# Kernel optimization log

Measured on AMD Instinct MI355X. Metric: run time of the kernel, lower is better.

The kernel has to match this reference:

```python
import jax, jax.numpy as jnp
import numpy as np

N_NODES = 50000
N_EDGES = 800000
N_GRAPHS = 64
F_IN, F_HID, F_OUT = 128, 128, 16


def _graph_conv(x, W, b, src, dst, activation=None):
    """DGL GraphConv with norm='both': D_out^{-1/2} A^T D_in^{-1/2} X W + b."""
    n = x.shape[0]
    ones = jnp.ones((src.shape[0],), dtype=x.dtype)
    deg_out = jnp.clip(jax.ops.segment_sum(ones, src, num_segments=n), 1.0)
    deg_in = jnp.clip(jax.ops.segment_sum(ones, dst, num_segments=n), 1.0)
    h = x * jax.lax.rsqrt(deg_out)[:, None]          # scale by src out-degree
    agg = jax.ops.segment_sum(h[src], dst, num_segments=n)  # gather+scatter-add
    agg = agg * jax.lax.rsqrt(deg_in)[:, None]       # scale by dst in-degree
    out = agg @ W + b
    if activation is not None:
        out = activation(out)
    return out


def setup_inputs() -> dict:
    key = jax.random.key(0)
    ks = jax.random.split(key, 6)
    x = jax.random.normal(ks[0], (N_NODES, F_IN), dtype=jnp.float32)
    W1 = jax.random.normal(ks[1], (F_IN, F_HID), dtype=jnp.float32) * (F_IN ** -0.5)
    b1 = jnp.zeros((F_HID,), dtype=jnp.float32)
    W2 = jax.random.normal(ks[2], (F_HID, F_OUT), dtype=jnp.float32) * (F_HID ** -0.5)
    b2 = jnp.zeros((F_OUT,), dtype=jnp.float32)
    src = jax.random.randint(ks[3], (N_EDGES,), 0, N_NODES, dtype=jnp.int32)
    dst = jax.random.randint(ks[4], (N_EDGES,), 0, N_NODES, dtype=jnp.int32)
    graph_ids = jnp.sort(jax.random.randint(ks[5], (N_NODES,), 0, N_GRAPHS, dtype=jnp.int32))
    return {"x": x, "W1": W1, "b1": b1, "W2": W2, "b2": b2,
            "src": src, "dst": dst, "graph_ids": graph_ids}


def reference(x, W1, b1, W2, b2, src, dst, graph_ids):
    h = _graph_conv(x, W1, b1, src, dst, activation=jax.nn.relu)
    h = _graph_conv(h, W2, b2, src, dst, activation=None)
    # dgl.mean_nodes: per-graph mean over nodes
    sums = jax.ops.segment_sum(h, graph_ids, num_segments=N_GRAPHS)
    counts = jnp.clip(jax.ops.segment_sum(jnp.ones((N_NODES,), h.dtype), graph_ids,
                                          num_segments=N_GRAPHS), 1.0)
    return sums / counts[:, None]
```

## Files before the change

### kernel.cpp

```cpp
#include <hip/hip_runtime.h>
#include <hip/hip_bf16.h>

#define N_NODES_C 50000
#define N_EDGES_C 800000
#define N_GRAPHS_C 64
#define NBKT 782
#define BKTP 784
#define CHUNK 4096
#define NBLK_E 196

typedef __attribute__((ext_vector_type(8))) short bf16x8;
typedef __attribute__((ext_vector_type(4))) float f32x4;

__device__ __forceinline__ unsigned short f2bf(float f) {
    unsigned u = __float_as_uint(f);
    unsigned r = (u + 0x7FFFu + ((u >> 16) & 1u)) >> 16;
    return (unsigned short)r;
}

__global__ __launch_bounds__(256) void k_hist(
    const int* __restrict__ src, const int* __restrict__ dst,
    int* __restrict__ hmatD, int* __restrict__ hmatS, int nE)
{
    __shared__ int hD[BKTP], hS[BKTP];
    const int tid = threadIdx.x, blk = blockIdx.x;
    for (int i = tid; i < BKTP; i += 256) { hD[i] = 0; hS[i] = 0; }
    __syncthreads();
    const int base = blk * CHUNK;
    for (int i = tid; i < CHUNK; i += 256) {
        int e = base + i;
        if (e < nE) {
            atomicAdd(&hD[dst[e] >> 6], 1);
            atomicAdd(&hS[src[e] >> 6], 1);
        }
    }
    __syncthreads();
    for (int i = tid; i < BKTP; i += 256) {
        hmatD[blk * BKTP + i] = hD[i];
        hmatS[blk * BKTP + i] = hS[i];
    }
}

__global__ __launch_bounds__(1024) void k_bscan(
    const int* __restrict__ hmatD, const int* __restrict__ hmatS,
    int* __restrict__ bbaseD, int* __restrict__ bbaseS,
    float* __restrict__ accbuf)
{
    __shared__ int part[1024];
    const int tid = threadIdx.x;
    const int* hm = blockIdx.x ? hmatS : hmatD;
    int* bb = blockIdx.x ? bbaseS : bbaseD;
    if (blockIdx.x == 0) accbuf[tid] = 0.f;
    int v = 0;
    if (tid < NBKT)
        for (int blk = 0; blk < NBLK_E; ++blk) v += hm[blk * BKTP + tid];
    part[tid] = v;
    __syncthreads();
    for (int off = 1; off < 1024; off <<= 1) {
        int t = (tid >= off) ? part[tid - off] : 0;
        __syncthreads();
        part[tid] += t;
        __syncthreads();
    }
    if (tid < NBKT) bb[tid] = part[tid] - v;
    if (tid == NBKT - 1) bb[NBKT] = part[tid];
}

__global__ __launch_bounds__(256) void k_boff(
    const int* __restrict__ hmatD, const int* __restrict__ hmatS,
    const int* __restrict__ bbaseD, const int* __restrict__ bbaseS,
    int* __restrict__ offmatD, int* __restrict__ offmatS)
{
    __shared__ int part[256];
    const int b = blockIdx.x, tid = threadIdx.x;
    const int* hm = blockIdx.y ? hmatS : hmatD;
    const int* bb = blockIdx.y ? bbaseS : bbaseD;
    int* om = blockIdx.y ? offmatS : offmatD;
    int v = (tid < NBLK_E) ? hm[tid * BKTP + b] : 0;
    part[tid] = v;
    __syncthreads();
    for (int off = 1; off < 256; off <<= 1) {
        int t = (tid >= off) ? part[tid - off] : 0;
        __syncthreads();
        part[tid] += t;
        __syncthreads();
    }
    if (tid < NBLK_E) om[tid * BKTP + b] = bb[b] + part[tid] - v;
}

__global__ __launch_bounds__(256) void k_scat(
    const int* __restrict__ src, const int* __restrict__ dst,
    const int* __restrict__ offmatD, const int* __restrict__ offmatS,
    unsigned* __restrict__ ed, unsigned char* __restrict__ es, int nE)
{
    __shared__ int curD[BKTP], curS[BKTP];
    const int tid = threadIdx.x, blk = blockIdx.x;
    for (int i = tid; i < BKTP; i += 256) {
        curD[i] = offmatD[blk * BKTP + i];
        curS[i] = offmatS[blk * BKTP + i];
    }
    __syncthreads();
    const int base = blk * CHUNK;
    for (int i = tid; i < CHUNK; i += 256) {
        int e = base + i;
        if (e < nE) {
            unsigned s = (unsigned)src[e], d = (unsigned)dst[e];
            int pD = atomicAdd(&curD[d >> 6], 1);
            ed[pD] = (d << 16) | s;
            int pS = atomicAdd(&curS[s >> 6], 1);
            es[pS] = (unsigned char)(s & 63u);
        }
    }
}

__global__ __launch_bounds__(256) void k_bucket(
    const unsigned* __restrict__ ed, const unsigned char* __restrict__ es,
    const int* __restrict__ bbaseD, const int* __restrict__ bbaseS,
    int* __restrict__ rowptr, float* __restrict__ rsI, float* __restrict__ rsO,
    unsigned short* __restrict__ csr_src, int nV)
{
    __shared__ int cnt[64], cur[64];
    const int tid = threadIdx.x;
    const int side = (blockIdx.x >= NBKT);
    const int b = side ? blockIdx.x - NBKT : blockIdx.x;

    if (tid < 64) cnt[tid] = 0;
    __syncthreads();

    if (!side) {
        const int lo = bbaseD[b], hi = bbaseD[b + 1];
        for (int j = lo + tid; j < hi; j += 256)
            atomicAdd(&cnt[(ed[j] >> 16) & 63u], 1);
        __syncthreads();
        if (tid < 64) {
            int c = cnt[tid];
            int v = c;
#pragma unroll
            for (int off = 1; off < 64; off <<= 1) {
                int n = __shfl_up(v, off, 64);
                if (tid >= off) v += n;
            }
            int excl = v - c;
            int node = b * 64 + tid;
            if (node <= nV) rowptr[node] = lo + excl;
            if (node < nV) rsI[node] = rsqrtf((float)max(c, 1));
            cur[tid] = excl;
        }
        __syncthreads();
        for (int j = lo + tid; j < hi; j += 256) {
            unsigned v = ed[j];
            int p = atomicAdd(&cur[(v >> 16) & 63u], 1);
            csr_src[lo + p] = (unsigned short)(v & 0xFFFFu);
        }
    } else {
        const int lo = bbaseS[b], hi = bbaseS[b + 1];
        for (int j = lo + tid; j < hi; j += 256)
            atomicAdd(&cnt[es[j]], 1);
        __syncthreads();
        if (tid < 64) {
            int node = b * 64 + tid;
            if (node < nV) rsO[node] = rsqrtf((float)max(cnt[tid], 1));
        }
    }
}

__global__ __launch_bounds__(256) void k_prepw(
    const float* __restrict__ x, const float* __restrict__ rsO,
    const float* __restrict__ W1, const float* __restrict__ W2,
    unsigned short* __restrict__ xs, unsigned short* __restrict__ w1f,
    unsigned short* __restrict__ w2f, int nV)
{
    const int tid = threadIdx.x;
    if (blockIdx.x < 6250) {
        int t = blockIdx.x * 256 + tid;
        if (t >= nV * 32) return;
        int v = t >> 5, q = t & 31;
        float w = rsO[v];
        float4 a = ((const float4*)(x + (size_t)v * 128))[q];
        ushort4 o;
        o.x = f2bf(a.x * w); o.y = f2bf(a.y * w);
        o.z = f2bf(a.z * w); o.w = f2bf(a.w * w);
        ((ushort4*)(xs + (size_t)v * 128))[q] = o;
        return;
    }
    int t = (blockIdx.x - 6250) * 256 + tid;
    if (t < 2048) {
        int kk = t >> 9, nt = (t >> 6) & 7, l = t & 63;
        int kb = kk * 32 + ((l >> 4) << 3), n = nt * 16 + (l & 15);
        ushort4 lo, hi;
        lo.x = f2bf(W1[(kb + 0) * 128 + n]); lo.y = f2bf(W1[(kb + 1) * 128 + n]);
        lo.z = f2bf(W1[(kb + 2) * 128 + n]); lo.w = f2bf(W1[(kb + 3) * 128 + n]);
        hi.x = f2bf(W1[(kb + 4) * 128 + n]); hi.y = f2bf(W1[(kb + 5) * 128 + n]);
        hi.z = f2bf(W1[(kb + 6) * 128 + n]); hi.w = f2bf(W1[(kb + 7) * 128 + n]);
        ((ushort4*)(w1f + t * 8))[0] = lo;
        ((ushort4*)(w1f + t * 8))[1] = hi;
    } else if (t < 2304) {
        int t2 = t - 2048;
        int kk = t2 >> 6, l = t2 & 63;
        int kb = kk * 32 + ((l >> 4) << 3), n = l & 15;
        ushort4 lo, hi;
        lo.x = f2bf(W2[(kb + 0) * 16 + n]); lo.y = f2bf(W2[(kb + 1) * 16 + n]);
        lo.z = f2bf(W2[(kb + 2) * 16 + n]); lo.w = f2bf(W2[(kb + 3) * 16 + n]);
        hi.x = f2bf(W2[(kb + 4) * 16 + n]); hi.y = f2bf(W2[(kb + 5) * 16 + n]);
        hi.z = f2bf(W2[(kb + 6) * 16 + n]); hi.w = f2bf(W2[(kb + 7) * 16 + n]);
        ((ushort4*)(w2f + t2 * 8))[0] = lo;
        ((ushort4*)(w2f + t2 * 8))[1] = hi;
    }
}

#define ACC8(vv)                                         \
    acc[0] += __uint_as_float((vv).x << 16);             \
    acc[1] += __uint_as_float((vv).x & 0xFFFF0000u);     \
    acc[2] += __uint_as_float((vv).y << 16);             \
    acc[3] += __uint_as_float((vv).y & 0xFFFF0000u);     \
    acc[4] += __uint_as_float((vv).z << 16);             \
    acc[5] += __uint_as_float((vv).z & 0xFFFF0000u);     \
    acc[6] += __uint_as_float((vv).w << 16);             \
    acc[7] += __uint_as_float((vv).w & 0xFFFF0000u);

__global__ __launch_bounds__(256) void k_agg1b(
    const unsigned short* __restrict__ xs, const int* __restrict__ rowptr,
    const unsigned short* __restrict__ csr_src, const float* __restrict__ rsI,
    unsigned short* __restrict__ agg1b, int nV)
{
    long long t = (long long)blockIdx.x * blockDim.x + threadIdx.x;
    int v = (int)(t >> 6);
    int lane = (int)(t & 63);
    if (v >= nV) return;
    int g = lane >> 4, fl = lane & 15;
    int beg = rowptr[v], end = rowptr[v + 1];
    float acc[8];
#pragma unroll
    for (int k = 0; k < 8; ++k) acc[k] = 0.f;

    int j = beg + g;
    while (j + 12 < end) {
        int s0 = csr_src[j], s1 = csr_src[j + 4], s2 = csr_src[j + 8], s3 = csr_src[j + 12];
        uint4 w0 = *(const uint4*)(xs + (size_t)s0 * 128 + fl * 8);
        uint4 w1 = *(const uint4*)(xs + (size_t)s1 * 128 + fl * 8);
        uint4 w2 = *(const uint4*)(xs + (size_t)s2 * 128 + fl * 8);
        uint4 w3 = *(const uint4*)(xs + (size_t)s3 * 128 + fl * 8);
        ACC8(w0); ACC8(w1); ACC8(w2); ACC8(w3);
        j += 16;
    }
    while (j + 4 < end) {
        int s0 = csr_src[j], s1 = csr_src[j + 4];
        uint4 w0 = *(const uint4*)(xs + (size_t)s0 * 128 + fl * 8);
        uint4 w1 = *(const uint4*)(xs + (size_t)s1 * 128 + fl * 8);
        ACC8(w0); ACC8(w1);
        j += 8;
    }
    if (j < end) {
        int s = csr_src[j];
        uint4 w0 = *(const uint4*)(xs + (size_t)s * 128 + fl * 8);
        ACC8(w0);
    }
#pragma unroll
    for (int k = 0; k < 8; ++k) {
        acc[k] += __shfl_xor(acc[k], 16, 64);
        acc[k] += __shfl_xor(acc[k], 32, 64);
    }
    float ri = rsI[v];
    if (g < 2) {
        ushort4 o;
        o.x = f2bf(acc[g * 4 + 0] * ri);
        o.y = f2bf(acc[g * 4 + 1] * ri);
        o.z = f2bf(acc[g * 4 + 2] * ri);
        o.w = f2bf(acc[g * 4 + 3] * ri);
        *(ushort4*)(agg1b + (size_t)v * 128 + fl * 8 + g * 4) = o;
    }
}

__global__ __launch_bounds__(256) void k_mfma(
    const unsigned short* __restrict__ agg1b, const float* __restrict__ b1,
    const unsigned short* __restrict__ w1f, const unsigned short* __restrict__ w2f,
    const float* __restrict__ rsO, unsigned short* __restrict__ y, int nV)
{
    __shared__ __align__(16) unsigned short h1[64 * 136];
    const int tid = threadIdx.x;
    const int w = tid >> 6, l = tid & 63;
    const int lr = l & 15, lg = l >> 4;
    const int row0 = blockIdx.x * 64;

    bf16x8 a[4];
    const unsigned short* abase = agg1b + (size_t)(row0 + w * 16 + lr) * 128 + lg * 8;
#pragma unroll
    for (int kk = 0; kk < 4; ++kk)
        a[kk] = *(const bf16x8*)(abase + kk * 32);

    f32x4 acc[8];
#pragma unroll
    for (int nt = 0; nt < 8; ++nt) acc[nt] = (f32x4){0.f, 0.f, 0.f, 0.f};

#pragma unroll
    for (int nt = 0; nt < 8; ++nt)
#pragma unroll
        for (int kk = 0; kk < 4; ++kk) {
            bf16x8 b = *(const bf16x8*)(w1f + ((kk * 8 + nt) * 64 + l) * 8);
            acc[nt] = __builtin_amdgcn_mfma_f32_16x16x32_bf16(a[kk], b, acc[nt], 0, 0, 0);
        }

#pragma unroll
    for (int nt = 0; nt < 8; ++nt) {
        float bb = b1[nt * 16 + lr];
#pragma unroll
        for (int i = 0; i < 4; ++i) {
            float h = fmaxf(acc[nt][i] + bb, 0.f);
            h1[(w * 16 + lg * 4 + i) * 136 + nt * 16 + lr] = f2bf(h);
        }
    }
    __syncthreads();

    f32x4 acc2 = (f32x4){0.f, 0.f, 0.f, 0.f};
#pragma unroll
    for (int kk = 0; kk < 4; ++kk) {
        bf16x8 a2 = *(const bf16x8*)(&h1[(w * 16 + lr) * 136 + kk * 32 + lg * 8]);
        bf16x8 b2 = *(const bf16x8*)(w2f + (kk * 64 + l) * 8);
        acc2 = __builtin_amdgcn_mfma_f32_16x16x32_bf16(a2, b2, acc2, 0, 0, 0);
    }
#pragma unroll
    for (int i = 0; i < 4; ++i) {
        int r = row0 + w * 16 + lg * 4 + i;
        if (r < nV) y[(size_t)r * 16 + lr] = f2bf(acc2[i] * rsO[r]);
    }
}

__global__ __launch_bounds__(256) void k_agg2p(
    const unsigned short* __restrict__ y, const int* __restrict__ rowptr,
    const unsigned short* __restrict__ csr_src, const float* __restrict__ rsI,
    const int* __restrict__ gid, float* __restrict__ accbuf, int nV)
{
    const int tid = threadIdx.x;
    const int lane = tid & 63, f = lane & 15, g4 = lane >> 4;
    const int wid = blockIdx.x * 4 + (tid >> 6);
    int v0 = wid * 8;
    if (v0 >= nV) return;
    int vend = min(v0 + 8, nV);
    float racc = 0.f;
    int curg = gid[v0];
    for (int v = v0; v < vend; ++v) {
        int beg = rowptr[v], end = rowptr[v + 1];
        float acc = 0.f;
        int j = beg + g4;
        while (j + 4 < end) {
            int s0 = csr_src[j], s1 = csr_src[j + 4];
            unsigned u0 = y[(size_t)s0 * 16 + f];
            unsigned u1 = y[(size_t)s1 * 16 + f];
            acc += __uint_as_float(u0 << 16) + __uint_as_float(u1 << 16);
            j += 8;
        }
        if (j < end) {
            unsigned u = y[(size_t)csr_src[j] * 16 + f];
            acc += __uint_as_float(u << 16);
        }
        acc += __shfl_xor(acc, 16, 64);
        acc += __shfl_xor(acc, 32, 64);
        int gg = gid[v];
        if (gg != curg) {
            if (g4 == 0 && racc != 0.f) unsafeAtomicAdd(&accbuf[curg * 16 + f], racc);
            racc = 0.f;
            curg = gg;
        }
        racc += acc * rsI[v];
    }
    if (g4 == 0 && racc != 0.f) unsafeAtomicAdd(&accbuf[curg * 16 + f], racc);
}

__device__ __forceinline__ int lowerb(const int* __restrict__ a, int n, int key) {
    int lo = 0, hi = n;
    while (lo < hi) { int m = (lo + hi) >> 1; if (a[m] < key) lo = m + 1; else hi = m; }
    return lo;
}

__global__ __launch_bounds__(256) void k_fin(
    const float* __restrict__ accbuf, const int* __restrict__ gid,
    const float* __restrict__ b2, float* __restrict__ out, int nV)
{
    int t = threadIdx.x;
    int g = t >> 2, f0 = (t & 3) * 4;
    int lo = lowerb(gid, nV, g);
    int hi = lowerb(gid, nV, g + 1);
    int n = hi - lo;
    float inv = (n > 0) ? 1.f / (float)n : 0.f;
#pragma unroll
    for (int k = 0; k < 4; ++k) {
        int f = f0 + k;
        out[g * 16 + f] = (n > 0) ? accbuf[g * 16 + f] * inv + b2[f] : 0.f;
    }
}

extern "C" void kernel_launch(void* const* d_in, const int* in_sizes, int n_in,
                              void* d_out, int out_size, void* d_ws, size_t ws_size,
                              hipStream_t stream) {
    const float* x   = (const float*)d_in[0];
    const float* W1  = (const float*)d_in[1];
    const float* b1  = (const float*)d_in[2];
    const float* W2  = (const float*)d_in[3];
    const float* b2  = (const float*)d_in[4];
    const int*   src = (const int*)d_in[5];
    const int*   dst = (const int*)d_in[6];
    const int*   gid = (const int*)d_in[7];
    float* out = (float*)d_out;

    int* p = (int*)d_ws;
    int*   bbaseD  = p;            p += 800;
    int*   bbaseS  = p;            p += 800;
    int*   rowptr  = p;            p += 50432;
    float* rsO     = (float*)p;    p += 50176;
    float* rsI     = (float*)p;    p += 50176;
    unsigned short* csr_src = (unsigned short*)p; p += 400128;
    unsigned short* w1f = (unsigned short*)p;     p += 8192;
    unsigned short* w2f = (unsigned short*)p;     p += 1024;
    unsigned short* y   = (unsigned short*)p;     p += 401408;
    float* accbuf  = (float*)p;    p += 1024;
    int*   BIG     = p;
    int*   hmatD   = BIG;
    int*   hmatS   = BIG + 153664;
    int*   offmatD = BIG + 307328;
    int*   offmatS = BIG + 460992;
    unsigned*      ed = (unsigned*)(BIG + 614656);
    unsigned char* es = (unsigned char*)(BIG + 1414656);
    unsigned short* xs    = (unsigned short*)BIG;
    unsigned short* agg1b = (unsigned short*)(BIG + 3211264);

    k_hist <<<NBLK_E, 256, 0, stream>>>(src, dst, hmatD, hmatS, N_EDGES_C);
    k_bscan<<<2, 1024, 0, stream>>>(hmatD, hmatS, bbaseD, bbaseS, accbuf);
    k_boff <<<dim3(NBKT, 2), 256, 0, stream>>>(hmatD, hmatS, bbaseD, bbaseS, offmatD, offmatS);
    k_scat <<<NBLK_E, 256, 0, stream>>>(src, dst, offmatD, offmatS, ed, es, N_EDGES_C);
    k_bucket<<<2 * NBKT, 256, 0, stream>>>(ed, es, bbaseD, bbaseS, rowptr, rsI, rsO, csr_src, N_NODES_C);

    k_prepw<<<6259, 256, 0, stream>>>(x, rsO, W1, W2, xs, w1f, w2f, N_NODES_C);
    k_agg1b<<<(N_NODES_C * 64 + 255) / 256, 256, 0, stream>>>(xs, rowptr, csr_src, rsI, agg1b, N_NODES_C);
    k_mfma <<<(N_NODES_C + 63) / 64, 256, 0, stream>>>(agg1b, b1, w1f, w2f, rsO, y, N_NODES_C);
    k_agg2p<<<(N_NODES_C + 31) / 32, 256, 0, stream>>>(y, rowptr, csr_src, rsI, gid, accbuf, N_NODES_C);
    k_fin  <<<1, 256, 0, stream>>>(accbuf, gid, b2, out, N_NODES_C);
}
```

Measured before the change: 127.8 us.

## Fuse layer-1 aggregation with MFMA GEMMs and fold x scaling into bucket kernel

Merges the edge-aggregation kernel and the MFMA GEMM kernel into one, so each block gathers 64 rows into LDS and runs both matmuls without a global round trip of agg1b. The x prescale and bf16 conversion moves into the source-degree side of k_bucket, and the weight repacking moves into k_boff, removing the k_prepw launch. Each wave now handles 16 nodes one after another, with one node per wave at a time. The grid shrinks to 782 blocks, which lowers the number of gathers in flight and may hurt latency hiding. The workspace layout is changed so xs no longer overlaps the sort scratch buffers.

```diff
diff --git a/kernel.cpp b/kernel.cpp
--- a/kernel.cpp
+++ b/kernel.cpp
@@ -69,7 +69,9 @@
 __global__ __launch_bounds__(256) void k_boff(
     const int* __restrict__ hmatD, const int* __restrict__ hmatS,
     const int* __restrict__ bbaseD, const int* __restrict__ bbaseS,
-    int* __restrict__ offmatD, int* __restrict__ offmatS)
+    int* __restrict__ offmatD, int* __restrict__ offmatS,
+    const float* __restrict__ W1, const float* __restrict__ W2,
+    unsigned short* __restrict__ w1f, unsigned short* __restrict__ w2f)
 {
     __shared__ int part[256];
     const int b = blockIdx.x, tid = threadIdx.x;
@@ -86,6 +88,32 @@
         __syncthreads();
     }
     if (tid < NBLK_E) om[tid * BKTP + b] = bb[b] + part[tid] - v;
+
+    if (blockIdx.y == 1 && b < 9) {
+        int t = b * 256 + tid;
+        if (t < 2048) {
+            int kk = t >> 9, nt = (t >> 6) & 7, l = t & 63;
+            int kb = kk * 32 + ((l >> 4) << 3), n = nt * 16 + (l & 15);
+            ushort4 lo, hi;
+            lo.x = f2bf(W1[(kb + 0) * 128 + n]); lo.y = f2bf(W1[(kb + 1) * 128 + n]);
+            lo.z = f2bf(W1[(kb + 2) * 128 + n]); lo.w = f2bf(W1[(kb + 3) * 128 + n]);
+            hi.x = f2bf(W1[(kb + 4) * 128 + n]); hi.y = f2bf(W1[(kb + 5) * 128 + n]);
+            hi.z = f2bf(W1[(kb + 6) * 128 + n]); hi.w = f2bf(W1[(kb + 7) * 128 + n]);
+            ((ushort4*)(w1f + t * 8))[0] = lo;
+            ((ushort4*)(w1f + t * 8))[1] = hi;
+        } else if (t < 2304) {
+            int t2 = t - 2048;
+            int kk = t2 >> 6, l = t2 & 63;
+            int kb = kk * 32 + ((l >> 4) << 3), n = l & 15;
+            ushort4 lo, hi;
+            lo.x = f2bf(W2[(kb + 0) * 16 + n]); lo.y = f2bf(W2[(kb + 1) * 16 + n]);
+            lo.z = f2bf(W2[(kb + 2) * 16 + n]); lo.w = f2bf(W2[(kb + 3) * 16 + n]);
+            hi.x = f2bf(W2[(kb + 4) * 16 + n]); hi.y = f2bf(W2[(kb + 5) * 16 + n]);
+            hi.z = f2bf(W2[(kb + 6) * 16 + n]); hi.w = f2bf(W2[(kb + 7) * 16 + n]);
+            ((ushort4*)(w2f + t2 * 8))[0] = lo;
+            ((ushort4*)(w2f + t2 * 8))[1] = hi;
+        }
+    }
 }
 
 __global__ __launch_bounds__(256) void k_scat(
@@ -116,10 +144,12 @@
 __global__ __launch_bounds__(256) void k_bucket(
     const unsigned* __restrict__ ed, const unsigned char* __restrict__ es,
     const int* __restrict__ bbaseD, const int* __restrict__ bbaseS,
+    const float* __restrict__ x,
     int* __restrict__ rowptr, float* __restrict__ rsI, float* __restrict__ rsO,
-    unsigned short* __restrict__ csr_src, int nV)
+    unsigned short* __restrict__ csr_src, unsigned short* __restrict__ xs, int nV)
 {
     __shared__ int cnt[64], cur[64];
+    __shared__ float rs[64];
     const int tid = threadIdx.x;
     const int side = (blockIdx.x >= NBKT);
     const int b = side ? blockIdx.x - NBKT : blockIdx.x;
@@ -159,52 +189,23 @@
         __syncthreads();
         if (tid < 64) {
             int node = b * 64 + tid;
-            if (node < nV) rsO[node] = rsqrtf((float)max(cnt[tid], 1));
-        }
-    }
-}
-
-__global__ __launch_bounds__(256) void k_prepw(
-    const float* __restrict__ x, const float* __restrict__ rsO,
-    const float* __restrict__ W1, const float* __restrict__ W2,
-    unsigned short* __restrict__ xs, unsigned short* __restrict__ w1f,
-    unsigned short* __restrict__ w2f, int nV)
-{
-    const int tid = threadIdx.x;
-    if (blockIdx.x < 6250) {
-        int t = blockIdx.x * 256 + tid;
-        if (t >= nV * 32) return;
-        int v = t >> 5, q = t & 31;
-        float w = rsO[v];
-        float4 a = ((const float4*)(x + (size_t)v * 128))[q];
-        ushort4 o;
-        o.x = f2bf(a.x * w); o.y = f2bf(a.y * w);
-        o.z = f2bf(a.z * w); o.w = f2bf(a.w * w);
-        ((ushort4*)(xs + (size_t)v * 128))[q] = o;
-        return;
-    }
-    int t = (blockIdx.x - 6250) * 256 + tid;
-    if (t < 2048) {
-        int kk = t >> 9, nt = (t >> 6) & 7, l = t & 63;
-        int kb = kk * 32 + ((l >> 4) << 3), n = nt * 16 + (l & 15);
-        ushort4 lo, hi;
-        lo.x = f2bf(W1[(kb + 0) * 128 + n]); lo.y = f2bf(W1[(kb + 1) * 128 + n]);
-        lo.z = f2bf(W1[(kb + 2) * 128 + n]); lo.w = f2bf(W1[(kb + 3) * 128 + n]);
-        hi.x = f2bf(W1[(kb + 4) * 128 + n]); hi.y = f2bf(W1[(kb + 5) * 128 + n]);
-        hi.z = f2bf(W1[(kb + 6) * 128 + n]); hi.w = f2bf(W1[(kb + 7) * 128 + n]);
-        ((ushort4*)(w1f + t * 8))[0] = lo;
-        ((ushort4*)(w1f + t * 8))[1] = hi;
-    } else if (t < 2304) {
-        int t2 = t - 2048;
-        int kk = t2 >> 6, l = t2 & 63;
-        int kb = kk * 32 + ((l >> 4) << 3), n = l & 15;
-        ushort4 lo, hi;
-        lo.x = f2bf(W2[(kb + 0) * 16 + n]); lo.y = f2bf(W2[(kb + 1) * 16 + n]);
-        lo.z = f2bf(W2[(kb + 2) * 16 + n]); lo.w = f2bf(W2[(kb + 3) * 16 + n]);
-        hi.x = f2bf(W2[(kb + 4) * 16 + n]); hi.y = f2bf(W2[(kb + 5) * 16 + n]);
-        hi.z = f2bf(W2[(kb + 6) * 16 + n]); hi.w = f2bf(W2[(kb + 7) * 16 + n]);
-        ((ushort4*)(w2f + t2 * 8))[0] = lo;
-        ((ushort4*)(w2f + t2 * 8))[1] = hi;
+            float r = rsqrtf((float)max(cnt[tid], 1));
+            if (node < nV) rsO[node] = r;
+            rs[tid] = r;
+        }
+        __syncthreads();
+        for (int q = tid; q < 64 * 32; q += 256) {
+            int n = q >> 5, c = q & 31;
+            int node = b * 64 + n;
+            if (node < nV) {
+                float wgt = rs[n];
+                float4 a = ((const float4*)(x + (size_t)node * 128))[c];
+                ushort4 o;
+                o.x = f2bf(a.x * wgt); o.y = f2bf(a.y * wgt);
+                o.z = f2bf(a.z * wgt); o.w = f2bf(a.w * wgt);
+                ((ushort4*)(xs + (size_t)node * 128))[c] = o;
+            }
+        }
     }
 }
 
@@ -218,86 +219,82 @@
     acc[6] += __uint_as_float((vv).w << 16);             \
     acc[7] += __uint_as_float((vv).w & 0xFFFF0000u);
 
-__global__ __launch_bounds__(256) void k_agg1b(
+__global__ __launch_bounds__(256) void k_fused(
     const unsigned short* __restrict__ xs, const int* __restrict__ rowptr,
     const unsigned short* __restrict__ csr_src, const float* __restrict__ rsI,
-    unsigned short* __restrict__ agg1b, int nV)
-{
-    long long t = (long long)blockIdx.x * blockDim.x + threadIdx.x;
-    int v = (int)(t >> 6);
-    int lane = (int)(t & 63);
-    if (v >= nV) return;
-    int g = lane >> 4, fl = lane & 15;
-    int beg = rowptr[v], end = rowptr[v + 1];
-    float acc[8];
-#pragma unroll
-    for (int k = 0; k < 8; ++k) acc[k] = 0.f;
-
-    int j = beg + g;
-    while (j + 12 < end) {
-        int s0 = csr_src[j], s1 = csr_src[j + 4], s2 = csr_src[j + 8], s3 = csr_src[j + 12];
-        uint4 w0 = *(const uint4*)(xs + (size_t)s0 * 128 + fl * 8);
-        uint4 w1 = *(const uint4*)(xs + (size_t)s1 * 128 + fl * 8);
-        uint4 w2 = *(const uint4*)(xs + (size_t)s2 * 128 + fl * 8);
-        uint4 w3 = *(const uint4*)(xs + (size_t)s3 * 128 + fl * 8);
-        ACC8(w0); ACC8(w1); ACC8(w2); ACC8(w3);
-        j += 16;
-    }
-    while (j + 4 < end) {
-        int s0 = csr_src[j], s1 = csr_src[j + 4];
-        uint4 w0 = *(const uint4*)(xs + (size_t)s0 * 128 + fl * 8);
-        uint4 w1 = *(const uint4*)(xs + (size_t)s1 * 128 + fl * 8);
-        ACC8(w0); ACC8(w1);
-        j += 8;
-    }
-    if (j < end) {
-        int s = csr_src[j];
-        uint4 w0 = *(const uint4*)(xs + (size_t)s * 128 + fl * 8);
-        ACC8(w0);
-    }
-#pragma unroll
-    for (int k = 0; k < 8; ++k) {
-        acc[k] += __shfl_xor(acc[k], 16, 64);
-        acc[k] += __shfl_xor(acc[k], 32, 64);
-    }
-    float ri = rsI[v];
-    if (g < 2) {
-        ushort4 o;
-        o.x = f2bf(acc[g * 4 + 0] * ri);
-        o.y = f2bf(acc[g * 4 + 1] * ri);
-        o.z = f2bf(acc[g * 4 + 2] * ri);
-        o.w = f2bf(acc[g * 4 + 3] * ri);
-        *(ushort4*)(agg1b + (size_t)v * 128 + fl * 8 + g * 4) = o;
-    }
-}
-
-__global__ __launch_bounds__(256) void k_mfma(
-    const unsigned short* __restrict__ agg1b, const float* __restrict__ b1,
-    const unsigned short* __restrict__ w1f, const unsigned short* __restrict__ w2f,
-    const float* __restrict__ rsO, unsigned short* __restrict__ y, int nV)
-{
-    __shared__ __align__(16) unsigned short h1[64 * 136];
+    const float* __restrict__ b1, const unsigned short* __restrict__ w1f,
+    const unsigned short* __restrict__ w2f, const float* __restrict__ rsO,
+    unsigned short* __restrict__ y, int nV)
+{
+    __shared__ __align__(16) unsigned short Al[64 * 136];
     const int tid = threadIdx.x;
     const int w = tid >> 6, l = tid & 63;
-    const int lr = l & 15, lg = l >> 4;
+    const int g = l >> 4, fl = l & 15;
     const int row0 = blockIdx.x * 64;
 
+    for (int n = 0; n < 16; ++n) {
+        int r = w * 16 + n;
+        int v = row0 + r;
+        float acc[8];
+#pragma unroll
+        for (int k = 0; k < 8; ++k) acc[k] = 0.f;
+        float ri = 0.f;
+        if (v < nV) {
+            ri = rsI[v];
+            int beg = rowptr[v], end = rowptr[v + 1];
+            int j = beg + g;
+            while (j + 12 < end) {
+                int s0 = csr_src[j], s1 = csr_src[j + 4], s2 = csr_src[j + 8], s3 = csr_src[j + 12];
+                uint4 w0 = *(const uint4*)(xs + (size_t)s0 * 128 + fl * 8);
+                uint4 w1 = *(const uint4*)(xs + (size_t)s1 * 128 + fl * 8);
+                uint4 w2 = *(const uint4*)(xs + (size_t)s2 * 128 + fl * 8);
+                uint4 w3 = *(const uint4*)(xs + (size_t)s3 * 128 + fl * 8);
+                ACC8(w0); ACC8(w1); ACC8(w2); ACC8(w3);
+                j += 16;
+            }
+            while (j + 4 < end) {
+                int s0 = csr_src[j], s1 = csr_src[j + 4];
+                uint4 w0 = *(const uint4*)(xs + (size_t)s0 * 128 + fl * 8);
+                uint4 w1 = *(const uint4*)(xs + (size_t)s1 * 128 + fl * 8);
+                ACC8(w0); ACC8(w1);
+                j += 8;
+            }
+            if (j < end) {
+                int s0 = csr_src[j];
+                uint4 w0 = *(const uint4*)(xs + (size_t)s0 * 128 + fl * 8);
+                ACC8(w0);
+            }
+        }
+#pragma unroll
+        for (int k = 0; k < 8; ++k) {
+            acc[k] += __shfl_xor(acc[k], 16, 64);
+            acc[k] += __shfl_xor(acc[k], 32, 64);
+        }
+        if (g < 2) {
+            ushort4 o;
+            o.x = f2bf(acc[g * 4 + 0] * ri);
+            o.y = f2bf(acc[g * 4 + 1] * ri);
+            o.z = f2bf(acc[g * 4 + 2] * ri);
+            o.w = f2bf(acc[g * 4 + 3] * ri);
+            *(ushort4*)(&Al[r * 136 + fl * 8 + g * 4]) = o;
+        }
+    }
+
+    const int lr = fl, lg = g;
     bf16x8 a[4];
-    const unsigned short* abase = agg1b + (size_t)(row0 + w * 16 + lr) * 128 + lg * 8;
 #pragma unroll
     for (int kk = 0; kk < 4; ++kk)
-        a[kk] = *(const bf16x8*)(abase + kk * 32);
-
-    f32x4 acc[8];
-#pragma unroll
-    for (int nt = 0; nt < 8; ++nt) acc[nt] = (f32x4){0.f, 0.f, 0.f, 0.f};
-
+        a[kk] = *(const bf16x8*)(&Al[(w * 16 + lr) * 136 + kk * 32 + lg * 8]);
+
+    f32x4 acc1[8];
+#pragma unroll
+    for (int nt = 0; nt < 8; ++nt) acc1[nt] = (f32x4){0.f, 0.f, 0.f, 0.f};
 #pragma unroll
     for (int nt = 0; nt < 8; ++nt)
 #pragma unroll
         for (int kk = 0; kk < 4; ++kk) {
             bf16x8 b = *(const bf16x8*)(w1f + ((kk * 8 + nt) * 64 + l) * 8);
-            acc[nt] = __builtin_amdgcn_mfma_f32_16x16x32_bf16(a[kk], b, acc[nt], 0, 0, 0);
+            acc1[nt] = __builtin_amdgcn_mfma_f32_16x16x32_bf16(a[kk], b, acc1[nt], 0, 0, 0);
         }
 
 #pragma unroll
@@ -305,16 +302,15 @@
         float bb = b1[nt * 16 + lr];
 #pragma unroll
         for (int i = 0; i < 4; ++i) {
-            float h = fmaxf(acc[nt][i] + bb, 0.f);
-            h1[(w * 16 + lg * 4 + i) * 136 + nt * 16 + lr] = f2bf(h);
-        }
-    }
-    __syncthreads();
+            float h = fmaxf(acc1[nt][i] + bb, 0.f);
+            Al[(w * 16 + lg * 4 + i) * 136 + nt * 16 + lr] = f2bf(h);
+        }
+    }
 
     f32x4 acc2 = (f32x4){0.f, 0.f, 0.f, 0.f};
 #pragma unroll
     for (int kk = 0; kk < 4; ++kk) {
-        bf16x8 a2 = *(const bf16x8*)(&h1[(w * 16 + lr) * 136 + kk * 32 + lg * 8]);
+        bf16x8 a2 = *(const bf16x8*)(&Al[(w * 16 + lr) * 136 + kk * 32 + lg * 8]);
         bf16x8 b2 = *(const bf16x8*)(w2f + (kk * 64 + l) * 8);
         acc2 = __builtin_amdgcn_mfma_f32_16x16x32_bf16(a2, b2, acc2, 0, 0, 0);
     }
@@ -413,25 +409,23 @@
     unsigned short* w2f = (unsigned short*)p;     p += 1024;
     unsigned short* y   = (unsigned short*)p;     p += 401408;
     float* accbuf  = (float*)p;    p += 1024;
-    int*   BIG     = p;
-    int*   hmatD   = BIG;
-    int*   hmatS   = BIG + 153664;
-    int*   offmatD = BIG + 307328;
-    int*   offmatS = BIG + 460992;
-    unsigned*      ed = (unsigned*)(BIG + 614656);
-    unsigned char* es = (unsigned char*)(BIG + 1414656);
-    unsigned short* xs    = (unsigned short*)BIG;
-    unsigned short* agg1b = (unsigned short*)(BIG + 3211264);
+    unsigned short* xs = (unsigned short*)p;      p += 3211264;
+    int*   hmatD   = p;            p += 153664;
+    int*   hmatS   = p;            p += 153664;
+    int*   offmatD = p;            p += 153664;
+    int*   offmatS = p;            p += 153664;
+    unsigned*      ed = (unsigned*)p;      p += 800000;
+    unsigned char* es = (unsigned char*)p; p += 200000;
 
     k_hist <<<NBLK_E, 256, 0, stream>>>(src, dst, hmatD, hmatS, N_EDGES_C);
     k_bscan<<<2, 1024, 0, stream>>>(hmatD, hmatS, bbaseD, bbaseS, accbuf);
-    k_boff <<<dim3(NBKT, 2), 256, 0, stream>>>(hmatD, hmatS, bbaseD, bbaseS, offmatD, offmatS);
+    k_boff <<<dim3(NBKT, 2), 256, 0, stream>>>(hmatD, hmatS, bbaseD, bbaseS,
+                                               offmatD, offmatS, W1, W2, w1f, w2f);
     k_scat <<<NBLK_E, 256, 0, stream>>>(src, dst, offmatD, offmatS, ed, es, N_EDGES_C);
-    k_bucket<<<2 * NBKT, 256, 0, stream>>>(ed, es, bbaseD, bbaseS, rowptr, rsI, rsO, csr_src, N_NODES_C);
-
-    k_prepw<<<6259, 256, 0, stream>>>(x, rsO, W1, W2, xs, w1f, w2f, N_NODES_C);
-    k_agg1b<<<(N_NODES_C * 64 + 255) / 256, 256, 0, stream>>>(xs, rowptr, csr_src, rsI, agg1b, N_NODES_C);
-    k_mfma <<<(N_NODES_C + 63) / 64, 256, 0, stream>>>(agg1b, b1, w1f, w2f, rsO, y, N_NODES_C);
+    k_bucket<<<2 * NBKT, 256, 0, stream>>>(ed, es, bbaseD, bbaseS, x,
+                                           rowptr, rsI, rsO, csr_src, xs, N_NODES_C);
+
+    k_fused<<<NBKT, 256, 0, stream>>>(xs, rowptr, csr_src, rsI, b1, w1f, w2f, rsO, y, N_NODES_C);
     k_agg2p<<<(N_NODES_C + 31) / 32, 256, 0, stream>>>(y, rowptr, csr_src, rsI, gid, accbuf, N_NODES_C);
     k_fin  <<<1, 256, 0, stream>>>(accbuf, gid, b2, out, N_NODES_C);
 }
```

Measured after the change: 133.3 us. 4.4% more time.
